# Kernel optimization log

Hardware: AMD Instinct MI355X
Metric: run time of the kernel (lower is better)

Reference implementation:

```python
import jax, jax.numpy as jnp
import numpy as np

N, K, M = 1024, 256, 1024
INIT_SCALE = 0.1


def setup_inputs() -> dict:
    key = jax.random.key(0)
    kx, kw = jax.random.split(key)
    x = jax.random.normal(kx, (N, K), dtype=jnp.float32)
    weight = jax.random.normal(kw, (M, K), dtype=jnp.float32) * INIT_SCALE
    return {"x": x, "weight": weight}


def reference(x, weight):
    # Tropical (max-plus) matmul: out[n, m] = max_k(|x[n, k]| + |w[m, k]|)
    ax = jnp.abs(x)        # [N, K]
    aw = jnp.abs(weight)   # [M, K]
    # broadcast to [N, M, K] then reduce over K (mirrors the original expand+add+max)
    return jnp.max(ax[:, None, :] + aw[None, :, :], axis=2)  # [N, M]
```

## Files before the change

kernel.cpp:

```cpp
#include <hip/hip_runtime.h>


typedef float v2f __attribute__((ext_vector_type(2)));
typedef float v4f __attribute__((ext_vector_type(4)));

constexpr int K    = 256;
constexpr int M    = 1024;
constexpr int TILE = 64;
constexpr int KP   = K / 2;
constexpr int P    = TILE;

__global__ void __launch_bounds__(256, 1)
tropical_kernel(const float* __restrict__ xg, const float* __restrict__ wg,
                float* __restrict__ outg)
{
    __shared__ __align__(16) v2f xs[KP * P];
    __shared__ __align__(16) v2f ws[KP * P];

    const int tid = threadIdx.x;
    const int tx  = tid & 15;
    const int ty  = tid >> 4;
    const int bn  = (int)(blockIdx.x >> 4) * TILE;
    const int bm  = (int)(blockIdx.x & 15) * TILE;

    const int r0 = tid >> 3;
    const int l  = tid & 7;

    const float* xr0 = xg + (bn + r0) * K;
    const float* xr1 = xg + (bn + r0 + 32) * K;
    const float* wr0 = wg + (bm + r0) * K;
    const float* wr1 = wg + (bm + r0 + 32) * K;

#pragma unroll
    for (int i = 0; i < 8; ++i) {
        const int q  = l + 8 * i;
        const int kp = 2 * q;
        v4f a = *(const v4f*)(xr0 + 4 * q);
        v4f b = *(const v4f*)(xr1 + 4 * q);
        v4f c = *(const v4f*)(wr0 + 4 * q);
        v4f d = *(const v4f*)(wr1 + 4 * q);
        const int s0 = ((kp    ) & 3) << 2;
        const int s1 = ((kp + 1) & 3) << 2;
        xs[(kp    ) * P + ((r0     ) ^ s0)] = (v2f){fabsf(a.x), fabsf(a.y)};
        xs[(kp + 1) * P + ((r0     ) ^ s1)] = (v2f){fabsf(a.z), fabsf(a.w)};
        xs[(kp    ) * P + ((r0 + 32) ^ s0)] = (v2f){fabsf(b.x), fabsf(b.y)};
        xs[(kp + 1) * P + ((r0 + 32) ^ s1)] = (v2f){fabsf(b.z), fabsf(b.w)};
        ws[(kp    ) * P + ((r0     ) ^ s0)] = (v2f){fabsf(c.x), fabsf(c.y)};
        ws[(kp + 1) * P + ((r0     ) ^ s1)] = (v2f){fabsf(c.z), fabsf(c.w)};
        ws[(kp    ) * P + ((r0 + 32) ^ s0)] = (v2f){fabsf(d.x), fabsf(d.y)};
        ws[(kp + 1) * P + ((r0 + 32) ^ s1)] = (v2f){fabsf(d.z), fabsf(d.w)};
    }

    __syncthreads();

    float acc[4][4];
#pragma unroll
    for (int a2 = 0; a2 < 4; ++a2)
#pragma unroll
        for (int b2 = 0; b2 < 4; ++b2) acc[a2][b2] = 0.f;

    int xo[4], wo[4];
#pragma unroll
    for (int c4 = 0; c4 < 4; ++c4) {
        xo[c4] = (4 * ty) ^ (c4 << 2);
        wo[c4] = (4 * tx) ^ (c4 << 2);
    }

#pragma unroll 4
    for (int kp = 0; kp < KP; ++kp) {
        const v2f* xrow = &xs[kp * P];
        const v2f* wrow = &ws[kp * P];
        const int xof = xo[kp & 3];
        const int wof = wo[kp & 3];
        v4f x01 = *(const v4f*)(xrow + xof);
        v4f x23 = *(const v4f*)(xrow + xof + 2);
        v4f w01 = *(const v4f*)(wrow + wof);
        v4f w23 = *(const v4f*)(wrow + wof + 2);

        v2f xa[4] = {{x01.x, x01.y}, {x01.z, x01.w},
                     {x23.x, x23.y}, {x23.z, x23.w}};
        v2f wa[4] = {{w01.x, w01.y}, {w01.z, w01.w},
                     {w23.x, w23.y}, {w23.z, w23.w}};

#pragma unroll
        for (int a2 = 0; a2 < 4; ++a2)
#pragma unroll
            for (int b2 = 0; b2 < 4; ++b2) {
                v2f s = xa[a2] + wa[b2];
                acc[a2][b2] = fmaxf(acc[a2][b2], fmaxf(s.x, s.y));
            }
    }

    const int n0 = bn + 4 * ty;
    const int m0 = bm + 4 * tx;
#pragma unroll
    for (int j = 0; j < 4; ++j) {
        v4f o = {acc[j][0], acc[j][1], acc[j][2], acc[j][3]};
        *(v4f*)(outg + (n0 + j) * M + m0) = o;
    }
}

extern "C" void kernel_launch(void* const* d_in, const int* in_sizes, int n_in,
                              void* d_out, int out_size, void* d_ws, size_t ws_size,
                              hipStream_t stream)
{
    const float* x = (const float*)d_in[0];
    const float* w = (const float*)d_in[1];
    float* out = (float*)d_out;

    dim3 grid(256);
    dim3 block(256);
    tropical_kernel<<<grid, block, 0, stream>>>(x, w, out);
}
```

Baseline: 72.57 us.

## Split K across two blocks with partial-max workspace and a merge kernel

The reduction dimension is split in half so 512 blocks each compute a partial max over 128 k values into a workspace slab, and a second kernel merges the two slabs with an elementwise max. This doubles the block count so more CUs are busy (256 blocks previously left part of a large GPU underfilled) and halves the shared memory per block so two blocks can share a CU. Each thread now owns a strided 4x4 output pattern read with scalar v2f shared loads using XOR swizzled indices. The cost is an extra kernel launch, 8 MB of partial-result writes plus reads, and uncoalesced scalar stores in place of vector stores.

```diff
diff --git a/kernel.cpp b/kernel.cpp
--- a/kernel.cpp
+++ b/kernel.cpp
@@ -5,50 +5,53 @@
 typedef float v4f __attribute__((ext_vector_type(4)));
 
 constexpr int K    = 256;
+constexpr int N    = 1024;
 constexpr int M    = 1024;
 constexpr int TILE = 64;
-constexpr int KP   = K / 2;
-constexpr int P    = TILE;
+constexpr int KH   = 128;
+constexpr int KPL  = KH / 2;
 
-__global__ void __launch_bounds__(256, 1)
-tropical_kernel(const float* __restrict__ xg, const float* __restrict__ wg,
-                float* __restrict__ outg)
+__global__ void __launch_bounds__(256, 2)
+tropical_main(const float* __restrict__ xg, const float* __restrict__ wg,
+              float* __restrict__ pw)
 {
-    __shared__ __align__(16) v2f xs[KP * P];
-    __shared__ __align__(16) v2f ws[KP * P];
+    __shared__ __align__(16) v2f xs[KPL * 64];
+    __shared__ __align__(16) v2f wsh[KPL * 64];
 
     const int tid = threadIdx.x;
     const int tx  = tid & 15;
     const int ty  = tid >> 4;
-    const int bn  = (int)(blockIdx.x >> 4) * TILE;
-    const int bm  = (int)(blockIdx.x & 15) * TILE;
+    const int bt  = (int)blockIdx.x & 255;
+    const int kh  = (int)blockIdx.x >> 8;
+    const int bn  = (bt >> 4) * TILE;
+    const int bm  = (bt & 15) * TILE;
+    const int k0  = kh * KH;
 
     const int r0 = tid >> 3;
     const int l  = tid & 7;
-
-    const float* xr0 = xg + (bn + r0) * K;
-    const float* xr1 = xg + (bn + r0 + 32) * K;
-    const float* wr0 = wg + (bm + r0) * K;
-    const float* wr1 = wg + (bm + r0 + 32) * K;
+    const v4f* x0 = (const v4f*)(xg + (bn + r0     ) * K + k0);
+    const v4f* x1 = (const v4f*)(xg + (bn + r0 + 32) * K + k0);
+    const v4f* w0 = (const v4f*)(wg + (bm + r0     ) * K + k0);
+    const v4f* w1 = (const v4f*)(wg + (bm + r0 + 32) * K + k0);
 
 #pragma unroll
-    for (int i = 0; i < 8; ++i) {
-        const int q  = l + 8 * i;
-        const int kp = 2 * q;
-        v4f a = *(const v4f*)(xr0 + 4 * q);
-        v4f b = *(const v4f*)(xr1 + 4 * q);
-        v4f c = *(const v4f*)(wr0 + 4 * q);
-        v4f d = *(const v4f*)(wr1 + 4 * q);
-        const int s0 = ((kp    ) & 3) << 2;
-        const int s1 = ((kp + 1) & 3) << 2;
-        xs[(kp    ) * P + ((r0     ) ^ s0)] = (v2f){fabsf(a.x), fabsf(a.y)};
-        xs[(kp + 1) * P + ((r0     ) ^ s1)] = (v2f){fabsf(a.z), fabsf(a.w)};
-        xs[(kp    ) * P + ((r0 + 32) ^ s0)] = (v2f){fabsf(b.x), fabsf(b.y)};
-        xs[(kp + 1) * P + ((r0 + 32) ^ s1)] = (v2f){fabsf(b.z), fabsf(b.w)};
-        ws[(kp    ) * P + ((r0     ) ^ s0)] = (v2f){fabsf(c.x), fabsf(c.y)};
-        ws[(kp + 1) * P + ((r0     ) ^ s1)] = (v2f){fabsf(c.z), fabsf(c.w)};
-        ws[(kp    ) * P + ((r0 + 32) ^ s0)] = (v2f){fabsf(d.x), fabsf(d.y)};
-        ws[(kp + 1) * P + ((r0 + 32) ^ s1)] = (v2f){fabsf(d.z), fabsf(d.w)};
+    for (int i = 0; i < 4; ++i) {
+        const int q   = l + 8 * i;
+        const int kpl = 2 * q;
+        v4f a = x0[q];
+        v4f b = x1[q];
+        v4f c = w0[q];
+        v4f d = w1[q];
+        const int s0 = ((kpl    ) & 3) << 2;
+        const int s1 = ((kpl + 1) & 3) << 2;
+        xs [(kpl    ) * 64 + ((r0     ) ^ s0)] = (v2f){fabsf(a.x), fabsf(a.y)};
+        xs [(kpl + 1) * 64 + ((r0     ) ^ s1)] = (v2f){fabsf(a.z), fabsf(a.w)};
+        xs [(kpl    ) * 64 + ((r0 + 32) ^ s0)] = (v2f){fabsf(b.x), fabsf(b.y)};
+        xs [(kpl + 1) * 64 + ((r0 + 32) ^ s1)] = (v2f){fabsf(b.z), fabsf(b.w)};
+        wsh[(kpl    ) * 64 + ((r0     ) ^ s0)] = (v2f){fabsf(c.x), fabsf(c.y)};
+        wsh[(kpl + 1) * 64 + ((r0     ) ^ s1)] = (v2f){fabsf(c.z), fabsf(c.w)};
+        wsh[(kpl    ) * 64 + ((r0 + 32) ^ s0)] = (v2f){fabsf(d.x), fabsf(d.y)};
+        wsh[(kpl + 1) * 64 + ((r0 + 32) ^ s1)] = (v2f){fabsf(d.z), fabsf(d.w)};
     }
 
     __syncthreads();
@@ -59,45 +62,51 @@
 #pragma unroll
         for (int b2 = 0; b2 < 4; ++b2) acc[a2][b2] = 0.f;
 
-    int xo[4], wo[4];
+    const int ty0 = ty;        const int tx0 = tx;
+    const int ty4 = ty ^ 4;    const int tx4 = tx ^ 4;
+    const int ty8 = ty ^ 8;    const int tx8 = tx ^ 8;
+    const int ty12 = ty ^ 12;  const int tx12 = tx ^ 12;
+
+#define PHASE(J, TYJ, TXJ)                                                   \
+    do {                                                                     \
+        const v2f* xr = xs  + (kp4 + (J)) * 64;                              \
+        const v2f* wr = wsh + (kp4 + (J)) * 64;                              \
+        v2f xa[4] = {xr[(TYJ)], xr[(TYJ) + 16], xr[(TYJ) + 32], xr[(TYJ) + 48]}; \
+        v2f wa[4] = {wr[(TXJ)], wr[(TXJ) + 16], wr[(TXJ) + 32], wr[(TXJ) + 48]}; \
+        _Pragma("unroll")                                                    \
+        for (int a2 = 0; a2 < 4; ++a2)                                       \
+            _Pragma("unroll")                                                \
+            for (int b2 = 0; b2 < 4; ++b2) {                                 \
+                v2f s = xa[a2] + wa[b2];                   \
+                acc[a2][b2] = fmaxf(acc[a2][b2], fmaxf(s.x, s.y)); \
+            }                                                                \
+    } while (0)
+
+    for (int kp4 = 0; kp4 < KPL; kp4 += 4) {
+        PHASE(0, ty0,  tx0);
+        PHASE(1, ty4,  tx4);
+        PHASE(2, ty8,  tx8);
+        PHASE(3, ty12, tx12);
+    }
+#undef PHASE
+
+    float* slab = pw + kh * (N * M);
 #pragma unroll
-    for (int c4 = 0; c4 < 4; ++c4) {
-        xo[c4] = (4 * ty) ^ (c4 << 2);
-        wo[c4] = (4 * tx) ^ (c4 << 2);
-    }
+    for (int a2 = 0; a2 < 4; ++a2)
+#pragma unroll
+        for (int b2 = 0; b2 < 4; ++b2)
+            slab[(bn + ty + 16 * a2) * M + (bm + tx + 16 * b2)] = acc[a2][b2];
+}
 
-#pragma unroll 4
-    for (int kp = 0; kp < KP; ++kp) {
-        const v2f* xrow = &xs[kp * P];
-        const v2f* wrow = &ws[kp * P];
-        const int xof = xo[kp & 3];
-        const int wof = wo[kp & 3];
-        v4f x01 = *(const v4f*)(xrow + xof);
-        v4f x23 = *(const v4f*)(xrow + xof + 2);
-        v4f w01 = *(const v4f*)(wrow + wof);
-        v4f w23 = *(const v4f*)(wrow + wof + 2);
-
-        v2f xa[4] = {{x01.x, x01.y}, {x01.z, x01.w},
-                     {x23.x, x23.y}, {x23.z, x23.w}};
-        v2f wa[4] = {{w01.x, w01.y}, {w01.z, w01.w},
-                     {w23.x, w23.y}, {w23.z, w23.w}};
-
-#pragma unroll
-        for (int a2 = 0; a2 < 4; ++a2)
-#pragma unroll
-            for (int b2 = 0; b2 < 4; ++b2) {
-                v2f s = xa[a2] + wa[b2];
-                acc[a2][b2] = fmaxf(acc[a2][b2], fmaxf(s.x, s.y));
-            }
-    }
-
-    const int n0 = bn + 4 * ty;
-    const int m0 = bm + 4 * tx;
-#pragma unroll
-    for (int j = 0; j < 4; ++j) {
-        v4f o = {acc[j][0], acc[j][1], acc[j][2], acc[j][3]};
-        *(v4f*)(outg + (n0 + j) * M + m0) = o;
-    }
+__global__ void __launch_bounds__(256)
+tropical_merge(const float* __restrict__ pw, float* __restrict__ outg)
+{
+    const int i = (int)blockIdx.x * 256 + (int)threadIdx.x;
+    v4f a = ((const v4f*)pw)[i];
+    v4f b = ((const v4f*)(pw + N * M))[i];
+    v4f m = {fmaxf(a.x, b.x), fmaxf(a.y, b.y),
+             fmaxf(a.z, b.z), fmaxf(a.w, b.w)};
+    ((v4f*)outg)[i] = m;
 }
 
 extern "C" void kernel_launch(void* const* d_in, const int* in_sizes, int n_in,
@@ -107,8 +116,8 @@
     const float* x = (const float*)d_in[0];
     const float* w = (const float*)d_in[1];
     float* out = (float*)d_out;
+    float* ws  = (float*)d_ws;
 
-    dim3 grid(256);
-    dim3 block(256);
-    tropical_kernel<<<grid, block, 0, stream>>>(x, w, out);
+    tropical_main<<<dim3(512), dim3(256), 0, stream>>>(x, w, ws);
+    tropical_merge<<<dim3(N * M / 4 / 256), dim3(256), 0, stream>>>(ws, out);
 }
```

After: 75.75 us. +4.4%, slower.
